# Kernel optimization log

Hardware: AMD Instinct MI355X
Metric: run time of the kernel (lower is better)

The kernel has to match this reference:

```python
import jax, jax.numpy as jnp
import numpy as np

E = 128       # estimators
R = 65536     # regions per estimator
S = 100000    # update samples


def setup_inputs() -> dict:
    key = jax.random.key(0)
    k1, k2, k3, k4, k5 = jax.random.split(key, 5)
    a = jax.random.uniform(k1, (E, R), dtype=jnp.float32) + 0.1
    b = jax.random.uniform(k2, (E, R), dtype=jnp.float32) + 0.1
    samples_regions = jax.random.randint(k3, (S, E), 0, R, dtype=jnp.int32)
    da = jax.random.uniform(k4, (S,), dtype=jnp.float32)
    db = jax.random.uniform(k5, (S,), dtype=jnp.float32)
    return {"a": a, "b": b, "samples_regions": samples_regions, "da": da, "db": db}


def reference(a, b, samples_regions, da, db):
    # Original: lax.scan over samples, each step vmapping over estimators and
    # doing beliefs.a.at[region].add(da). Addition is commutative, so the whole
    # scan is a single batched scatter-add into the [E, R] tables.
    est = jnp.arange(a.shape[0], dtype=samples_regions.dtype)[None, :]  # [1, E]
    new_a = a.at[est, samples_regions].add(da[:, None])  # indices broadcast to [S, E]
    new_b = b.at[est, samples_regions].add(db[:, None])
    return jnp.stack([new_a, new_b])  # [2, E, R]
```

## Files before the change

kernel.cpp:

```cpp
#include <hip/hip_runtime.h>

#define NE 128
#define NR 65536
#define NS 100000
#define NSP 100096
#define NG8 (NS / 8)
#define NG8_MAIN 12288

#define CHUNK4 32768
#define CHUNK 16384

#define FXS16   2048.0f
#define FXI16   4.8828125e-4f
#define FXQ16(vv) ((unsigned)__builtin_fmaf((vv), FXS16, 0.5f))

typedef float vfloat4 __attribute__((ext_vector_type(4)));
typedef unsigned short u16x8 __attribute__((ext_vector_type(8)));

__global__ __launch_bounds__(256) void EnsembleBeliefs_transpose16(
    const int* __restrict__ in,
    unsigned short* __restrict__ outT,
    const float* __restrict__ da,
    const float* __restrict__ db,
    unsigned* __restrict__ qv)
{
    __shared__ int tile[64 * 133];
    const int t  = threadIdx.x;
    const int s0 = blockIdx.x * 64;

    {
        const int idx = blockIdx.x * 256 + t;
        if (idx < NS / 4) {
            const float4 va = ((const float4*)da)[idx];
            const float4 vb = ((const float4*)db)[idx];
            uint4 q;
            q.x = FXQ16(va.x) | (FXQ16(vb.x) << 16);
            q.y = FXQ16(va.y) | (FXQ16(vb.y) << 16);
            q.z = FXQ16(va.z) | (FXQ16(vb.z) << 16);
            q.w = FXQ16(va.w) | (FXQ16(vb.w) << 16);
            ((uint4*)qv)[idx] = q;
        }
    }

#pragma unroll
    for (int k = 0; k < 8; ++k) {
        const int idx = k * 256 + t;
        const int sl  = idx >> 5;
        const int c4  = idx & 31;
        const int s   = s0 + sl;
        if (s < NS) {
            const int4 v = *(const int4*)(in + (size_t)s * NE + 4 * c4);
            const int o = sl * 133 + 4 * c4;
            tile[o] = v.x; tile[o + 1] = v.y; tile[o + 2] = v.z; tile[o + 3] = v.w;
        }
    }
    __syncthreads();

#pragma unroll
    for (int k = 0; k < 8; ++k) {
        const int idx = k * 256 + t;
        const int e = idx >> 4;
        const int c = idx & 15;
        const unsigned w0 = ((unsigned)tile[(4 * c + 0) * 133 + e] & 0xffffu) |
                            ((unsigned)tile[(4 * c + 1) * 133 + e] << 16);
        const unsigned w1 = ((unsigned)tile[(4 * c + 2) * 133 + e] & 0xffffu) |
                            ((unsigned)tile[(4 * c + 3) * 133 + e] << 16);
        *(uint2*)(outT + (size_t)e * NSP + s0 + 4 * c) = make_uint2(w0, w1);
    }
}

#define H5_AT(rr, qq)                                                          \
    { const int _rl = (int)(rr) - base;                                        \
      if ((unsigned)_rl < (unsigned)CHUNK4) atomicAdd(&h[_rl], (qq)); }

#define H5_GROUP(rv, q0, q1)                                                   \
    H5_AT(rv[0], (q0).x) H5_AT(rv[1], (q0).y) H5_AT(rv[2], (q0).z) H5_AT(rv[3], (q0).w) \
    H5_AT(rv[4], (q1).x) H5_AT(rv[5], (q1).y) H5_AT(rv[6], (q1).z) H5_AT(rv[7], (q1).w)

__global__ __launch_bounds__(1024) void EnsembleBeliefs_hist5(
    const unsigned short* __restrict__ regT,
    const unsigned* __restrict__ qv,
    const float* __restrict__ a,
    const float* __restrict__ b,
    float* __restrict__ out)
{
    extern __shared__ unsigned h[];
    const int e    = blockIdx.x;
    const int base = blockIdx.y << 15;
    const int tid  = threadIdx.x;

    const u16x8* reg8 = (const u16x8*)(regT + (size_t)e * NSP);
    const uint4* q4   = (const uint4*)qv;

    u16x8 rC  = reg8[tid];
    uint4 qC0 = q4[2 * tid];
    uint4 qC1 = q4[2 * tid + 1];

    uint4* h4 = (uint4*)h;
    for (int j = tid; j < CHUNK4 / 4; j += 1024) h4[j] = make_uint4(0u, 0u, 0u, 0u);
    __syncthreads();

    for (int k = 1; k < 12; ++k) {
        const int ip = tid + (k << 10);
        const u16x8 rN  = reg8[ip];
        const uint4 qN0 = q4[2 * ip];
        const uint4 qN1 = q4[2 * ip + 1];
        __builtin_amdgcn_sched_barrier(0);
        H5_GROUP(rC, qC0, qC1)
        rC = rN; qC0 = qN0; qC1 = qN1;
    }
    H5_GROUP(rC, qC0, qC1)

    if (tid < NG8 - NG8_MAIN) {
        const int ip = NG8_MAIN + tid;
        const u16x8 r  = reg8[ip];
        const uint4 t0 = q4[2 * ip];
        const uint4 t1 = q4[2 * ip + 1];
        H5_GROUP(r, t0, t1)
    }
    __syncthreads();

    const size_t off = ((size_t)e << 16) + (size_t)base;
    const vfloat4* srcA = (const vfloat4*)(a + off);
    const vfloat4* srcB = (const vfloat4*)(b + off);
    vfloat4* dstA = (vfloat4*)(out + off);
    vfloat4* dstB = (vfloat4*)(out + (((size_t)NE << 16)) + off);
    for (int j = tid; j < CHUNK4 / 4; j += 1024) {
        const uint4 x = h4[j];
        const vfloat4 sa = __builtin_nontemporal_load(srcA + j);
        const vfloat4 sb = __builtin_nontemporal_load(srcB + j);
        vfloat4 oa, ob;
        oa.x = __builtin_fmaf((float)(x.x & 0xffffu), FXI16, sa.x);
        ob.x = __builtin_fmaf((float)(x.x >> 16),     FXI16, sb.x);
        oa.y = __builtin_fmaf((float)(x.y & 0xffffu), FXI16, sa.y);
        ob.y = __builtin_fmaf((float)(x.y >> 16),     FXI16, sb.y);
        oa.z = __builtin_fmaf((float)(x.z & 0xffffu), FXI16, sa.z);
        ob.z = __builtin_fmaf((float)(x.z >> 16),     FXI16, sb.z);
        oa.w = __builtin_fmaf((float)(x.w & 0xffffu), FXI16, sa.w);
        ob.w = __builtin_fmaf((float)(x.w >> 16),     FXI16, sb.w);
        __builtin_nontemporal_store(oa, dstA + j);
        __builtin_nontemporal_store(ob, dstB + j);
    }
}

#define H5S_AT(rr, qq)                                                         \
    { const int _rl = (int)(rr) - base;                                        \
      if ((unsigned)_rl < (unsigned)CHUNK) atomicAdd(&hs[_rl], (qq)); }

__global__ __launch_bounds__(1024) void EnsembleBeliefs_hist5s(
    const unsigned short* __restrict__ regT,
    const unsigned* __restrict__ qv,
    const float* __restrict__ a,
    const float* __restrict__ b,
    float* __restrict__ out)
{
    __shared__ unsigned hs[CHUNK];
    const int e    = blockIdx.x;
    const int base = blockIdx.y << 14;
    const int tid  = threadIdx.x;

    uint4* h4 = (uint4*)hs;
    for (int j = tid; j < CHUNK / 4; j += 1024) h4[j] = make_uint4(0u, 0u, 0u, 0u);
    __syncthreads();

    const u16x8* reg8 = (const u16x8*)(regT + (size_t)e * NSP);
    const uint4* q4   = (const uint4*)qv;
    for (int i = tid; i < NG8; i += 1024) {
        const u16x8 r  = reg8[i];
        const uint4 t0 = q4[2 * i];
        const uint4 t1 = q4[2 * i + 1];
        H5S_AT(r[0], t0.x) H5S_AT(r[1], t0.y) H5S_AT(r[2], t0.z) H5S_AT(r[3], t0.w)
        H5S_AT(r[4], t1.x) H5S_AT(r[5], t1.y) H5S_AT(r[6], t1.z) H5S_AT(r[7], t1.w)
    }
    __syncthreads();

    const size_t off = ((size_t)e << 16) + (size_t)base;
    const vfloat4* srcA = (const vfloat4*)(a + off);
    const vfloat4* srcB = (const vfloat4*)(b + off);
    vfloat4* dstA = (vfloat4*)(out + off);
    vfloat4* dstB = (vfloat4*)(out + (((size_t)NE << 16)) + off);
    for (int j = tid; j < CHUNK / 4; j += 1024) {
        const uint4 x = h4[j];
        const vfloat4 sa = __builtin_nontemporal_load(srcA + j);
        const vfloat4 sb = __builtin_nontemporal_load(srcB + j);
        vfloat4 oa, ob;
        oa.x = __builtin_fmaf((float)(x.x & 0xffffu), FXI16, sa.x);
        ob.x = __builtin_fmaf((float)(x.x >> 16),     FXI16, sb.x);
        oa.y = __builtin_fmaf((float)(x.y & 0xffffu), FXI16, sa.y);
        ob.y = __builtin_fmaf((float)(x.y >> 16),     FXI16, sb.y);
        oa.z = __builtin_fmaf((float)(x.z & 0xffffu), FXI16, sa.z);
        ob.z = __builtin_fmaf((float)(x.z >> 16),     FXI16, sb.z);
        oa.w = __builtin_fmaf((float)(x.w & 0xffffu), FXI16, sa.w);
        ob.w = __builtin_fmaf((float)(x.w >> 16),     FXI16, sb.w);
        __builtin_nontemporal_store(oa, dstA + j);
        __builtin_nontemporal_store(ob, dstB + j);
    }
}

__global__ __launch_bounds__(256) void EnsembleBeliefs_scatter(
    const int* __restrict__ regions,
    const float* __restrict__ da,
    const float* __restrict__ db,
    float* __restrict__ out)
{
    const int idx = blockIdx.x * 256 + threadIdx.x;
    const int s = idx >> 7;
    const int e = idx & (NE - 1);
    const int region = regions[idx];
    const size_t off = ((size_t)e << 16) + (size_t)region;
    atomicAdd(out + off, da[s]);
    atomicAdd(out + ((size_t)NE << 16) + off, db[s]);
}

extern "C" void kernel_launch(void* const* d_in, const int* in_sizes, int n_in,
                              void* d_out, int out_size, void* d_ws, size_t ws_size,
                              hipStream_t stream) {
    const float* a       = (const float*)d_in[0];
    const float* b       = (const float*)d_in[1];
    const int*   regions = (const int*)  d_in[2];
    const float* da      = (const float*)d_in[3];
    const float* db      = (const float*)d_in[4];
    float* out = (float*)d_out;

    const size_t regT16_bytes = (size_t)NE * NSP * sizeof(unsigned short);
    const size_t qv_bytes     = (size_t)NS * sizeof(unsigned);

    if (ws_size >= regT16_bytes + qv_bytes) {
        unsigned short* regT16 = (unsigned short*)d_ws;
        unsigned*       qv     = (unsigned*)((char*)d_ws + regT16_bytes);

        EnsembleBeliefs_transpose16<<<(NS + 63) / 64, 256, 0, stream>>>(
            regions, regT16, da, db, qv);

        static int big_lds = -1;
        if (big_lds < 0) {
            big_lds = (hipFuncSetAttribute(
                           reinterpret_cast<const void*>(EnsembleBeliefs_hist5),
                           hipFuncAttributeMaxDynamicSharedMemorySize,
                           CHUNK4 * (int)sizeof(unsigned)) == hipSuccess) ? 1 : 0;
        }

        if (big_lds) {
            dim3 hgrid(NE, 2);
            EnsembleBeliefs_hist5<<<hgrid, 1024, CHUNK4 * sizeof(unsigned), stream>>>(
                regT16, qv, a, b, out);
        } else {
            dim3 hgrid(NE, 4);
            EnsembleBeliefs_hist5s<<<hgrid, 1024, 0, stream>>>(regT16, qv, a, b, out);
        }
    } else {
        const size_t tbl_elems = (size_t)NE * NR;
        (void)hipMemcpyAsync(out, a, tbl_elems * sizeof(float), hipMemcpyDeviceToDevice, stream);
        (void)hipMemcpyAsync(out + tbl_elems, b, tbl_elems * sizeof(float), hipMemcpyDeviceToDevice, stream);
        EnsembleBeliefs_scatter<<<(NS * NE) / 256, 256, 0, stream>>>(regions, da, db, out);
    }
}
```

Baseline: 172.4 us.

## Swizzle transpose tile with wider stores and deepen histogram prefetch to two

The transpose kernel's padded shared tile is replaced by an XOR-swizzled 128-wide layout, so rows are written with single 16-byte LDS stores and each thread emits 16-byte (8-sample) global stores instead of 8-byte ones. The histogram kernel now keeps two groups of region/value loads in flight ahead of the atomic-add work instead of one. The aim is fewer LDS bank conflicts and instructions in the transpose, and better hiding of global load latency behind LDS atomics. In exchange the histogram kernel holds more registers, which could affect occupancy at 1024 threads, and the swizzle adds index arithmetic.

```diff
diff --git a/kernel.cpp b/kernel.cpp
--- a/kernel.cpp
+++ b/kernel.cpp
@@ -24,7 +24,7 @@
     const float* __restrict__ db,
     unsigned* __restrict__ qv)
 {
-    __shared__ int tile[64 * 133];
+    __shared__ int tile[64 * 128];
     const int t  = threadIdx.x;
     const int s0 = blockIdx.x * 64;
 
@@ -50,22 +50,29 @@
         const int s   = s0 + sl;
         if (s < NS) {
             const int4 v = *(const int4*)(in + (size_t)s * NE + 4 * c4);
-            const int o = sl * 133 + 4 * c4;
-            tile[o] = v.x; tile[o + 1] = v.y; tile[o + 2] = v.z; tile[o + 3] = v.w;
+            const int swz = c4 ^ (sl & 31) ^ ((sl >> 3) & 7);
+            *(int4*)&tile[sl * 128 + 4 * swz] = v;
         }
     }
     __syncthreads();
 
 #pragma unroll
-    for (int k = 0; k < 8; ++k) {
-        const int idx = k * 256 + t;
-        const int e = idx >> 4;
-        const int c = idx & 15;
-        const unsigned w0 = ((unsigned)tile[(4 * c + 0) * 133 + e] & 0xffffu) |
-                            ((unsigned)tile[(4 * c + 1) * 133 + e] << 16);
-        const unsigned w1 = ((unsigned)tile[(4 * c + 2) * 133 + e] & 0xffffu) |
-                            ((unsigned)tile[(4 * c + 3) * 133 + e] << 16);
-        *(uint2*)(outT + (size_t)e * NSP + s0 + 4 * c) = make_uint2(w0, w1);
+    for (int k = 0; k < 4; ++k) {
+        const int u  = k * 256 + t;
+        const int c3 = u & 7;
+        const int e  = u >> 3;
+        const int ec = e >> 2;
+        const int ew = e & 3;
+        unsigned w[4];
+#pragma unroll
+        for (int p = 0; p < 4; ++p) {
+            const int r0 = 8 * c3 + 2 * p;
+            const int r1 = r0 + 1;
+            const unsigned lo = (unsigned)tile[r0 * 128 + 4 * (ec ^ (r0 & 31) ^ ((r0 >> 3) & 7)) + ew] & 0xffffu;
+            const unsigned hi = (unsigned)tile[r1 * 128 + 4 * (ec ^ (r1 & 31) ^ ((r1 >> 3) & 7)) + ew] << 16;
+            w[p] = lo | hi;
+        }
+        *(uint4*)(outT + (size_t)e * NSP + s0 + 8 * c3) = make_uint4(w[0], w[1], w[2], w[3]);
     }
 }
 
@@ -92,24 +99,29 @@
     const u16x8* reg8 = (const u16x8*)(regT + (size_t)e * NSP);
     const uint4* q4   = (const uint4*)qv;
 
-    u16x8 rC  = reg8[tid];
-    uint4 qC0 = q4[2 * tid];
-    uint4 qC1 = q4[2 * tid + 1];
+    u16x8 rA  = reg8[tid];
+    uint4 qA0 = q4[2 * tid];
+    uint4 qA1 = q4[2 * tid + 1];
+    u16x8 rB  = reg8[tid + 1024];
+    uint4 qB0 = q4[2 * (tid + 1024)];
+    uint4 qB1 = q4[2 * (tid + 1024) + 1];
 
     uint4* h4 = (uint4*)h;
     for (int j = tid; j < CHUNK4 / 4; j += 1024) h4[j] = make_uint4(0u, 0u, 0u, 0u);
     __syncthreads();
 
-    for (int k = 1; k < 12; ++k) {
+    for (int k = 2; k < 12; ++k) {
         const int ip = tid + (k << 10);
         const u16x8 rN  = reg8[ip];
         const uint4 qN0 = q4[2 * ip];
         const uint4 qN1 = q4[2 * ip + 1];
         __builtin_amdgcn_sched_barrier(0);
-        H5_GROUP(rC, qC0, qC1)
-        rC = rN; qC0 = qN0; qC1 = qN1;
-    }
-    H5_GROUP(rC, qC0, qC1)
+        H5_GROUP(rA, qA0, qA1)
+        rA = rB; qA0 = qB0; qA1 = qB1;
+        rB = rN; qB0 = qN0; qB1 = qN1;
+    }
+    H5_GROUP(rA, qA0, qA1)
+    H5_GROUP(rB, qB0, qB1)
 
     if (tid < NG8 - NG8_MAIN) {
         const int ip = NG8_MAIN + tid;
```

After: 173.7 us. No clear change (+0.8%).
